# Kernel tuning notes

Hardware: AMD Instinct MI355X
Metric: run time of the kernel (lower is better)

## Reference

```python
import jax, jax.numpy as jnp
import numpy as np

# --- problem-size constants (uniform instance of the ragged structure) ---
B = 64            # claims
EVI = 5           # evidence sequences per claim
SEQS = B * EVI    # total PLM sequences
L = 256           # tokens per sequence
D = 768           # in_channels (PLM hidden)
WORDS = 32        # word-nodes per evidence
TPW = 4           # token refs averaged per word (word_select mean)
N = B * EVI * WORDS   # total graph nodes = 10240
E = N * 16            # edges
R = 4                 # num_relations
DOUT = 768            # out_channels
LH = 1024             # linear_hidden_channels
NC = 3                # num_class


def setup_inputs() -> dict:
    key = jax.random.key(0)
    ks = jax.random.split(key, 16)
    s = 0.02
    return {
        "token_feats": jax.random.normal(ks[0], (SEQS, L, D), jnp.float32),
        "concat_cls": jax.random.normal(ks[1], (B, D), jnp.float32),
        "W_rel1": jax.random.normal(ks[2], (R, D, D), jnp.float32) * s,
        "W_root1": jax.random.normal(ks[3], (D, D), jnp.float32) * s,
        "b1": jnp.zeros((D,), jnp.float32),
        "W_rel2": jax.random.normal(ks[4], (R, D, DOUT), jnp.float32) * s,
        "W_root2": jax.random.normal(ks[5], (D, DOUT), jnp.float32) * s,
        "b2": jnp.zeros((DOUT,), jnp.float32),
        "att_w0": jax.random.normal(ks[6], (D + 2 * DOUT, DOUT), jnp.float32) * s,
        "att_w1": jax.random.normal(ks[7], (DOUT, 1), jnp.float32) * s,
        "lin1_w": jax.random.normal(ks[8], (2 * DOUT + D, LH), jnp.float32) * s,
        "lin1_b": jnp.zeros((LH,), jnp.float32),
        "lin2_w": jax.random.normal(ks[9], (LH, NC), jnp.float32) * s,
        "lin2_b": jnp.zeros((NC,), jnp.float32),
        "word_token_idx": jax.random.randint(ks[10], (N * TPW,), 0, SEQS * L),
        "edge_index": jax.random.randint(ks[11], (2, E), 0, N),
        "edge_type": jax.random.randint(ks[12], (E,), 0, R),
        "claim_seq_idx": jnp.arange(B) * EVI,  # first sequence of each claim
    }


def _rgcn(x, edge_index, edge_type, W_rel, W_root, b):
    # PyG RGCNConv with mean aggregation per relation + root transform + bias
    xr = jnp.einsum('nd,rde->rne', x, W_rel)        # [R, N, Dout]
    src, dst = edge_index[0], edge_index[1]
    msg = xr[edge_type, src]                        # [E, Dout]
    seg = dst * R + edge_type                       # (target, relation) buckets
    cnt = jax.ops.segment_sum(jnp.ones((E,), x.dtype), seg, num_segments=N * R)
    msg = msg / jnp.maximum(cnt, 1.0)[seg][:, None]
    agg = jax.ops.segment_sum(msg, dst, num_segments=N)
    return agg + x @ W_root + b


def reference(token_feats, concat_cls, W_rel1, W_root1, b1, W_rel2, W_root2, b2,
              att_w0, att_w1, lin1_w, lin1_b, lin2_w, lin2_b,
              word_token_idx, edge_index, edge_type, claim_seq_idx):
    # word_select: mean of token vectors per word-node (TPW uniform here)
    tok = token_feats.reshape(-1, D)
    x = tok[word_token_idx].reshape(N, TPW, D).mean(axis=1)       # [N, D]
    claim_cls = token_feats[claim_seq_idx, 0, :]                  # [B, D]

    # 2 RGCN layers with ReLU
    x = jax.nn.relu(_rgcn(x, edge_index, edge_type, W_rel1, W_root1, b1))
    x = jax.nn.relu(_rgcn(x, edge_index, edge_type, W_rel2, W_root2, b2))

    # per-evidence mean||max pooling over its words (uniform WORDS per evidence)
    xe = x.reshape(B * EVI, WORDS, DOUT)
    ev = jnp.concatenate([xe.mean(axis=1), xe.max(axis=1)], axis=-1)  # [B*EVI, 2*Dout]

    # attention scores per evidence, conditioned on the claim CLS
    cc = jnp.repeat(claim_cls, EVI, axis=0)                       # [B*EVI, D]
    h = jax.nn.relu(jnp.concatenate([cc, ev], axis=-1) @ att_w0)
    p = h @ att_w1                                                # [B*EVI, 1]

    # per-claim softmax over its evidences, weighted sum of evidence reps
    a = jax.nn.softmax(p.reshape(B, EVI), axis=1)
    graph = jnp.einsum('be,bed->bd', a, ev.reshape(B, EVI, 2 * DOUT))  # [B, 2*Dout]

    rep = jnp.concatenate([graph, concat_cls], axis=-1)           # [B, 2*Dout + D]
    # dropout is identity in eval mode
    out = jax.nn.log_softmax(jax.nn.relu(rep @ lin1_w + lin1_b) @ lin2_w + lin2_b, axis=-1)
    attention = jax.nn.sigmoid(p[:, 0])                           # [B*EVI]
    return out, attention
```

## Files before the change

### kernel.cpp

```cpp
#include <hip/hip_runtime.h>
#include <hip/hip_fp16.h>


#define BN 64
#define EVI 5
#define SEQS (BN * EVI)
#define LSEQ 256
#define DIM 768
#define WORDS 32
#define TPW 4
#define NNODE (BN * EVI * WORDS)
#define NEDGE (NNODE * 16)
#define RREL 4
#define DOUT 768
#define LH 1024
#define NCLS 3
#define KBIG (5 * DIM)
#define KATT (DIM + 2 * DOUT)

typedef float f32x4 __attribute__((ext_vector_type(4)));
typedef __bf16 bf16x8 __attribute__((ext_vector_type(8)));
typedef unsigned short u16x4 __attribute__((ext_vector_type(4)));

__device__ inline unsigned short f2bf(float f) {
    union { float f; unsigned int u; } v; v.f = f;
    unsigned int u = v.u;
    unsigned int lsb = (u >> 16) & 1u;
    u += 0x7fffu + lsb;
    return (unsigned short)(u >> 16);
}
__device__ inline float bf2f(unsigned short h) {
    union { float f; unsigned int u; } v; v.u = ((unsigned int)h) << 16; return v.f;
}

__device__ inline float ldin(const void* p, long i, int f) {
    if (f == 1) return __half2float(((const __half*)p)[i]);
    if (f == 2) return bf2f(((const unsigned short*)p)[i]);
    return ((const float*)p)[i];
}

__global__ void detect_kernel(const void* w, int* flag) {
    const int lane = threadIdx.x;
    const unsigned int* u32 = (const unsigned int*)w;
    const unsigned short* u16 = (const unsigned short*)w;
    int tiny = 0;
    for (int i = lane; i < 2048; i += 64) {
        unsigned int b = u32[i];
        float f; __builtin_memcpy(&f, &b, 4);
        float a = fabsf(f);
        if (!(a > 1e-10f)) tiny++;
    }
    int band = 0;
    for (int i = lane; i < 4096; i += 64) {
        unsigned short h = u16[i];
        int e8 = (h >> 7) & 0xFF;
        if (h == 0 || (e8 >= 0x66 && e8 <= 0x86)) band++;
    }
#pragma unroll
    for (int o = 32; o > 0; o >>= 1) {
        tiny += __shfl_down(tiny, o);
        band += __shfl_down(band, o);
    }
    if (lane == 0) {
        if (tiny > 1024) { *flag = 1; return; }
        *flag = (band > 3900) ? 2 : 0;
    }
}

__global__ void convert_kernel(const void* __restrict__ src, float* __restrict__ dst,
                               long n, const int* __restrict__ flag)
{
    int f = *flag;
    long stride = (long)gridDim.x * 256;
    for (long i = (long)blockIdx.x * 256 + threadIdx.x; i < n; i += stride)
        dst[i] = ldin(src, i, f);
}

__global__ __launch_bounds__(256) void gather_mean_kernel(
    const void* __restrict__ tok, const int* __restrict__ widx,
    unsigned short* __restrict__ xb, const int* __restrict__ flag)
{
    int f = *flag;
    int n = blockIdx.x;
    long i0 = widx[n * 4 + 0], i1 = widx[n * 4 + 1];
    long i2 = widx[n * 4 + 2], i3 = widx[n * 4 + 3];
    for (int c = threadIdx.x; c < DIM; c += 256) {
        float s = ldin(tok, i0 * DIM + c, f) + ldin(tok, i1 * DIM + c, f)
                + ldin(tok, i2 * DIM + c, f) + ldin(tok, i3 * DIM + c, f);
        xb[(long)n * DIM + c] = f2bf(s * 0.25f);
    }
}

__global__ void count_kernel(const int* __restrict__ ei, const int* __restrict__ et,
                             int* __restrict__ cnt)
{
    int e = blockIdx.x * 256 + threadIdx.x;
    if (e >= NEDGE) return;
    int dst = ei[NEDGE + e];
    int r = et[e];
    atomicAdd(&cnt[dst * RREL + r], 1);
}

__global__ __launch_bounds__(1024) void scan_kernel(const int* __restrict__ cnt,
                                                    int* __restrict__ offs, int n)
{
    const int CH = (n + 1023) >> 10;
    int tid = threadIdx.x;
    int base = tid * CH;
    int s = 0;
    for (int i = 0; i < CH; i++)
        if (base + i < n) s += cnt[base + i];
    __shared__ int buf[1024];
    buf[tid] = s;
    __syncthreads();
    for (int o = 1; o < 1024; o <<= 1) {
        int t = (tid >= o) ? buf[tid - o] : 0;
        __syncthreads();
        buf[tid] += t;
        __syncthreads();
    }
    int run = (tid == 0) ? 0 : buf[tid - 1];
    if (tid == 0) offs[0] = 0;
    for (int i = 0; i < CH; i++) {
        if (base + i < n) {
            run += cnt[base + i];
            offs[base + i + 1] = run;
        }
    }
}

__global__ void fill_kernel(const int* __restrict__ ei, const int* __restrict__ et,
                            const int* __restrict__ offs, int* __restrict__ cursor,
                            int* __restrict__ sorted)
{
    int e = blockIdx.x * 256 + threadIdx.x;
    if (e >= NEDGE) return;
    int src = ei[e];
    int dst = ei[NEDGE + e];
    int r = et[e];
    int seg = dst * RREL + r;
    int pos = offs[seg] + atomicAdd(&cursor[seg], 1);
    sorted[pos] = src;
}

__global__ __launch_bounds__(768) void aggregate_kernel(
    const unsigned short* __restrict__ xsrc, long xstride,
    const int* __restrict__ offs, const int* __restrict__ sorted,
    unsigned short* __restrict__ A, int write_root)
{
    const int n = blockIdx.x;
    const int t = threadIdx.x;
    const int g = t / 192;
    const int l = t - g * 192;
    const long rs4 = xstride >> 2;
    const u16x4* __restrict__ xs4 = (const u16x4*)xsrc;
    u16x4* __restrict__ Ap = (u16x4*)A;
    const long baseQ = ((long)n * KBIG) >> 2;
    const int s0 = offs[n * RREL + g];
    const int s1 = offs[n * RREL + g + 1];
    const float inv = 1.0f / (float)max(s1 - s0, 1);
    float p0[4] = {0, 0, 0, 0}, p1[4] = {0, 0, 0, 0};
    float p2[4] = {0, 0, 0, 0}, p3[4] = {0, 0, 0, 0};
    int i = s0;
    for (; i + 3 < s1; i += 4) {
        int e0 = sorted[i], e1 = sorted[i + 1], e2 = sorted[i + 2], e3 = sorted[i + 3];
        u16x4 w0 = xs4[(long)e0 * rs4 + l];
        u16x4 w1 = xs4[(long)e1 * rs4 + l];
        u16x4 w2 = xs4[(long)e2 * rs4 + l];
        u16x4 w3 = xs4[(long)e3 * rs4 + l];
#pragma unroll
        for (int c = 0; c < 4; c++) {
            p0[c] += bf2f(w0[c]); p1[c] += bf2f(w1[c]);
            p2[c] += bf2f(w2[c]); p3[c] += bf2f(w3[c]);
        }
    }
    for (; i < s1; i++) {
        int e = sorted[i];
        u16x4 w = xs4[(long)e * rs4 + l];
#pragma unroll
        for (int c = 0; c < 4; c++) p0[c] += bf2f(w[c]);
    }
    u16x4 o;
#pragma unroll
    for (int c = 0; c < 4; c++)
        o[c] = f2bf(((p0[c] + p1[c]) + (p2[c] + p3[c])) * inv);
    Ap[baseQ + g * (DIM / 4) + l] = o;
    if (write_root && t < 192)
        Ap[baseQ + RREL * (DIM / 4) + t] = xs4[(long)n * rs4 + t];
}

__global__ __launch_bounds__(256) void transpose_cast_kernel(
    const void* __restrict__ in, int Ncols,
    unsigned short* __restrict__ out, int outStride, int colOff,
    const int* __restrict__ flag)
{
    int f = *flag;
    __shared__ float t[32][33];
    int kt = blockIdx.x * 32, nt = blockIdx.y * 32;
    int lx = threadIdx.x & 31, ly = threadIdx.x >> 5;
    for (int i = 0; i < 4; i++)
        t[ly + i * 8][lx] = ldin(in, (long)(kt + ly + i * 8) * Ncols + nt + lx, f);
    __syncthreads();
    for (int i = 0; i < 4; i++)
        out[(long)(nt + ly + i * 8) * outStride + colOff + kt + lx] = f2bf(t[lx][ly + i * 8]);
}

__global__ __launch_bounds__(256) void gemm_bt_kernel(
    const unsigned short* __restrict__ A, const unsigned short* __restrict__ Bt,
    int K, const float* __restrict__ bias, int relu,
    float* __restrict__ outF, long strideF,
    unsigned short* __restrict__ outB, long strideB)
{
    __shared__ __align__(16) unsigned short As[128 * 32];
    __shared__ __align__(16) unsigned short Bs[128 * 32];
    const int tid = threadIdx.x;
    const int lane = tid & 63, wv = tid >> 6;
    const int wr = wv >> 1, wc = wv & 1;
    const int lr = lane & 15, q = lane >> 4;
    const long m0 = (long)blockIdx.x * 128, n0 = (long)blockIdx.y * 128;

    f32x4 acc[4][4] = {};

    for (int kt = 0; kt < K; kt += 32) {
#pragma unroll
        for (int i = 0; i < 2; i++) {
            int chunk = i * 256 + tid;
            int row = chunk >> 2, kc = (chunk & 3) * 8;
            const unsigned short* ga = A + (m0 + row) * K + kt + kc;
            const unsigned short* gb = Bt + (n0 + row) * K + kt + kc;
            int ldsbase = (i * 256 + wv * 64) * 8;
            __builtin_amdgcn_global_load_lds(
                (const __attribute__((address_space(1))) void*)ga,
                (__attribute__((address_space(3))) void*)&As[ldsbase], 16, 0, 0);
            __builtin_amdgcn_global_load_lds(
                (const __attribute__((address_space(1))) void*)gb,
                (__attribute__((address_space(3))) void*)&Bs[ldsbase], 16, 0, 0);
        }
        __syncthreads();
        bf16x8 af[4], bfr[4];
#pragma unroll
        for (int i = 0; i < 4; i++)
            af[i] = *(const bf16x8*)&As[(wr * 64 + i * 16 + lr) * 32 + q * 8];
#pragma unroll
        for (int j = 0; j < 4; j++)
            bfr[j] = *(const bf16x8*)&Bs[(wc * 64 + j * 16 + lr) * 32 + q * 8];
#pragma unroll
        for (int i = 0; i < 4; i++)
#pragma unroll
            for (int j = 0; j < 4; j++)
                acc[i][j] = __builtin_amdgcn_mfma_f32_16x16x32_bf16(af[i], bfr[j], acc[i][j], 0, 0, 0);
        __syncthreads();
    }

#pragma unroll
    for (int i = 0; i < 4; i++) {
#pragma unroll
        for (int j = 0; j < 4; j++) {
            long col = n0 + wc * 64 + j * 16 + lr;
            float bv = bias ? bias[col] : 0.0f;
#pragma unroll
            for (int r = 0; r < 4; r++) {
                long row = m0 + wr * 64 + i * 16 + q * 4 + r;
                float v = acc[i][j][r] + bv;
                if (relu) v = fmaxf(v, 0.0f);
                if (outF) outF[row * strideF + col] = v;
                if (outB) outB[row * strideB + col] = f2bf(v);
            }
        }
    }
}

__global__ __launch_bounds__(256) void pool_cc_kernel(
    const float* __restrict__ C2, const void* __restrict__ tok,
    const int* __restrict__ csi, unsigned short* __restrict__ A3,
    float* __restrict__ evF, const int* __restrict__ flag)
{
    int f = *flag;
    int s = blockIdx.x;
    int b = s / EVI;
    long seq = csi[b];
    for (int c = threadIdx.x; c < DIM; c += 256) {
        float mx = -1e30f, sm = 0.0f;
        const float* col = C2 + (long)s * WORDS * DOUT + c;
        for (int w = 0; w < WORDS; w++) {
            float v = col[(long)w * DOUT];
            sm += v;
            mx = fmaxf(mx, v);
        }
        float mean = sm * (1.0f / WORDS);
        evF[(long)s * (2 * DOUT) + c] = mean;
        evF[(long)s * (2 * DOUT) + DOUT + c] = mx;
        A3[(long)s * KATT + c] = f2bf(ldin(tok, seq * LSEQ * DIM + c, f));
        A3[(long)s * KATT + DIM + c] = f2bf(mean);
        A3[(long)s * KATT + DIM + DOUT + c] = f2bf(mx);
    }
}

__global__ __launch_bounds__(256) void att_finish_kernel(
    const float* __restrict__ C3, const void* __restrict__ w1,
    const float* __restrict__ evF, const void* __restrict__ ccls,
    float* __restrict__ out, unsigned short* __restrict__ A4,
    const int* __restrict__ flag)
{
    int f = *flag;
    int b = blockIdx.x;
    int t = threadIdx.x;
    __shared__ float red[256];
    __shared__ float a[EVI];
    __shared__ float psh[EVI];
    for (int e = 0; e < EVI; e++) {
        int s = b * EVI + e;
        float sum = 0.0f;
        for (int k = t; k < DOUT; k += 256)
            sum += C3[(long)s * DOUT + k] * ldin(w1, k, f);
        red[t] = sum;
        __syncthreads();
        for (int o = 128; o > 0; o >>= 1) {
            if (t < o) red[t] += red[t + o];
            __syncthreads();
        }
        if (t == 0) psh[e] = red[0];
        __syncthreads();
    }
    if (t < EVI) out[BN * NCLS + b * EVI + t] = 1.0f / (1.0f + __expf(-psh[t]));
    if (t == 0) {
        float m = -1e30f;
        for (int e = 0; e < EVI; e++) m = fmaxf(m, psh[e]);
        float ssum = 0.0f, ex[EVI];
        for (int e = 0; e < EVI; e++) { ex[e] = __expf(psh[e] - m); ssum += ex[e]; }
        for (int e = 0; e < EVI; e++) a[e] = ex[e] / ssum;
    }
    __syncthreads();
    for (int d = t; d < 2 * DOUT; d += 256) {
        float gg = 0.0f;
        for (int e = 0; e < EVI; e++)
            gg += a[e] * evF[(long)(b * EVI + e) * (2 * DOUT) + d];
        A4[(long)b * KATT + d] = f2bf(gg);
    }
    for (int c = t; c < DIM; c += 256)
        A4[(long)b * KATT + 2 * DOUT + c] = f2bf(ldin(ccls, (long)b * DIM + c, f));
}

__global__ __launch_bounds__(256) void final_kernel(
    const float* __restrict__ C4, const void* __restrict__ w2,
    const void* __restrict__ bb, float* __restrict__ out,
    const int* __restrict__ flag)
{
    int f = *flag;
    int b = blockIdx.x;
    float s0 = 0.0f, s1 = 0.0f, s2 = 0.0f;
    for (int k = threadIdx.x; k < LH; k += 256) {
        float h = C4[(long)b * LH + k];
        s0 += h * ldin(w2, k * NCLS + 0, f);
        s1 += h * ldin(w2, k * NCLS + 1, f);
        s2 += h * ldin(w2, k * NCLS + 2, f);
    }
    __shared__ float r0[256], r1[256], r2[256];
    int t = threadIdx.x;
    r0[t] = s0; r1[t] = s1; r2[t] = s2;
    __syncthreads();
    for (int o = 128; o > 0; o >>= 1) {
        if (t < o) { r0[t] += r0[t + o]; r1[t] += r1[t + o]; r2[t] += r2[t + o]; }
        __syncthreads();
    }
    if (t == 0) {
        float l0 = r0[0] + ldin(bb, 0, f), l1 = r1[0] + ldin(bb, 1, f), l2 = r2[0] + ldin(bb, 2, f);
        float m = fmaxf(l0, fmaxf(l1, l2));
        float lse = logf(__expf(l0 - m) + __expf(l1 - m) + __expf(l2 - m)) + m;
        out[b * NCLS + 0] = l0 - lse;
        out[b * NCLS + 1] = l1 - lse;
        out[b * NCLS + 2] = l2 - lse;
    }
}

extern "C" void kernel_launch(void* const* d_in, const int* in_sizes, int n_in,
                              void* d_out, int out_size, void* d_ws, size_t ws_size,
                              hipStream_t stream)
{
    const void* tok      = d_in[0];
    const void* ccls_r   = d_in[1];
    const void* W_rel1_r = d_in[2];
    const void* W_root1_r= d_in[3];
    const void* b1_r     = d_in[4];
    const void* W_rel2_r = d_in[5];
    const void* W_root2_r= d_in[6];
    const void* b2_r     = d_in[7];
    const void* att_w0_r = d_in[8];
    const void* att_w1_r = d_in[9];
    const void* lin1_w_r = d_in[10];
    const void* lin1_b_r = d_in[11];
    const void* lin2_w_r = d_in[12];
    const void* lin2_b_r = d_in[13];
    const int* widx      = (const int*)d_in[14];
    const int* ei        = (const int*)d_in[15];
    const int* et        = (const int*)d_in[16];
    const int* csi       = (const int*)d_in[17];
    float* out           = (float*)d_out;

    char* ws = (char*)d_ws;
    size_t off = 0;
    auto alloc = [&](size_t bytes) { size_t o = off; off = (off + bytes + 255) & ~(size_t)255; return o; };

    int* flag   = (int*)(ws + alloc(256));
    float* b1F     = (float*)(ws + alloc((size_t)DIM * 4));
    float* b2F     = (float*)(ws + alloc((size_t)DOUT * 4));
    float* l1bF    = (float*)(ws + alloc((size_t)LH * 4));
    unsigned short* xb  = (unsigned short*)(ws + alloc((size_t)NNODE * DIM * 2));
    unsigned short* A1  = (unsigned short*)(ws + alloc((size_t)NNODE * KBIG * 2));
    unsigned short* X1  = (unsigned short*)(ws + alloc((size_t)NNODE * DOUT * 2));
    unsigned short* Wt1 = (unsigned short*)(ws + alloc((size_t)DIM * KBIG * 2));
    unsigned short* Wt2 = (unsigned short*)(ws + alloc((size_t)DIM * KBIG * 2));
    unsigned short* Wt3 = (unsigned short*)(ws + alloc((size_t)DOUT * KATT * 2));
    unsigned short* Wt4 = (unsigned short*)(ws + alloc((size_t)LH * KATT * 2));
    float* C2           = (float*)(ws + alloc((size_t)NNODE * DOUT * 4));
    unsigned short* A3  = (unsigned short*)(ws + alloc((size_t)384 * KATT * 2));
    float* C3           = (float*)(ws + alloc((size_t)384 * DOUT * 4));
    float* evF          = (float*)(ws + alloc((size_t)SEQS * 2 * DOUT * 4));
    unsigned short* A4  = (unsigned short*)(ws + alloc((size_t)128 * KATT * 2));
    float* C4           = (float*)(ws + alloc((size_t)128 * LH * 4));
    int* cnt            = (int*)(ws + alloc((size_t)2 * NNODE * RREL * 4));
    int* cursor         = cnt + NNODE * RREL;
    int* offs           = (int*)(ws + alloc((size_t)(NNODE * RREL + 1) * 4));
    int* sorted         = (int*)(ws + alloc((size_t)NEDGE * 4));
    (void)ws_size; (void)in_sizes; (void)n_in; (void)out_size;

    detect_kernel<<<1, 64, 0, stream>>>(W_rel1_r, flag);
    auto conv = [&](const void* src, float* dst, long n) {
        int grid = (int)min((n + 255) / 256, (long)2048);
        convert_kernel<<<grid, 256, 0, stream>>>(src, dst, n, flag);
    };
    conv(b1_r,     b1F,     DIM);
    conv(b2_r,     b2F,     DOUT);
    conv(lin1_b_r, l1bF,    LH);

    hipMemsetAsync(cnt, 0, (size_t)2 * NNODE * RREL * 4, stream);
    count_kernel<<<NEDGE / 256, 256, 0, stream>>>(ei, et, cnt);
    scan_kernel<<<1, 1024, 0, stream>>>(cnt, offs, NNODE * RREL);
    fill_kernel<<<NEDGE / 256, 256, 0, stream>>>(ei, et, offs, cursor, sorted);

    gather_mean_kernel<<<NNODE, 256, 0, stream>>>(tok, widx, xb, flag);

    transpose_cast_kernel<<<dim3(96, 24), 256, 0, stream>>>(W_rel1_r, DIM, Wt1, KBIG, 0, flag);
    transpose_cast_kernel<<<dim3(24, 24), 256, 0, stream>>>(W_root1_r, DIM, Wt1, KBIG, 4 * DIM, flag);
    transpose_cast_kernel<<<dim3(96, 24), 256, 0, stream>>>(W_rel2_r, DOUT, Wt2, KBIG, 0, flag);
    transpose_cast_kernel<<<dim3(24, 24), 256, 0, stream>>>(W_root2_r, DOUT, Wt2, KBIG, 4 * DIM, flag);
    transpose_cast_kernel<<<dim3(72, 24), 256, 0, stream>>>(att_w0_r, DOUT, Wt3, KATT, 0, flag);
    transpose_cast_kernel<<<dim3(72, 32), 256, 0, stream>>>(lin1_w_r, LH, Wt4, KATT, 0, flag);

    aggregate_kernel<<<NNODE, 768, 0, stream>>>(xb, DIM, offs, sorted, A1, 1);
    gemm_bt_kernel<<<dim3(NNODE / 128, DIM / 128), 256, 0, stream>>>(
        A1, Wt1, KBIG, b1F, 1, nullptr, 0, X1, DOUT);

    aggregate_kernel<<<NNODE, 768, 0, stream>>>(X1, DOUT, offs, sorted, A1, 1);
    gemm_bt_kernel<<<dim3(NNODE / 128, DOUT / 128), 256, 0, stream>>>(
        A1, Wt2, KBIG, b2F, 1, C2, DOUT, nullptr, 0);

    pool_cc_kernel<<<SEQS, 256, 0, stream>>>(C2, tok, csi, A3, evF, flag);
    gemm_bt_kernel<<<dim3(3, DOUT / 128), 256, 0, stream>>>(
        A3, Wt3, KATT, nullptr, 1, C3, DOUT, nullptr, 0);
    att_finish_kernel<<<BN, 256, 0, stream>>>(C3, att_w1_r, evF, ccls_r, out, A4, flag);

    gemm_bt_kernel<<<dim3(1, LH / 128), 256, 0, stream>>>(
        A4, Wt4, KATT, l1bF, 1, C4, LH, nullptr, 0);
    final_kernel<<<BN, 256, 0, stream>>>(C4, lin2_w_r, lin2_b_r, out, flag);
}
```

Baseline: 950.0 us.

## Batch weight transposes, split GEMM A operand, widen K tile, vectorize gather

Several changes land together. The three bias conversions and the six weight transpose launches are each merged into a single batched launch, which cuts launch overhead. The root-feature copy into the aggregate buffer is dropped; the GEMM now reads the root part of K directly from the node feature matrix through a second A pointer, saving a write and a read of one fifth of A. The GEMM K tile grows from 32 to 64, halving barrier count at the cost of doubled LDS use. gather_mean now uses one thread per 4 channels with float4 loads on the fp32 path.

```diff
diff --git a/kernel.cpp b/kernel.cpp
--- a/kernel.cpp
+++ b/kernel.cpp
@@ -15,6 +15,7 @@
 #define DOUT 768
 #define LH 1024
 #define NCLS 3
+#define KAGG (4 * DIM)
 #define KBIG (5 * DIM)
 #define KATT (DIM + 2 * DOUT)
 
@@ -67,28 +68,47 @@
     }
 }
 
-__global__ void convert_kernel(const void* __restrict__ src, float* __restrict__ dst,
-                               long n, const int* __restrict__ flag)
-{
-    int f = *flag;
-    long stride = (long)gridDim.x * 256;
-    for (long i = (long)blockIdx.x * 256 + threadIdx.x; i < n; i += stride)
-        dst[i] = ldin(src, i, f);
-}
-
-__global__ __launch_bounds__(256) void gather_mean_kernel(
+__global__ void convert3_kernel(const void* __restrict__ b1, const void* __restrict__ b2,
+                                const void* __restrict__ l1b,
+                                float* __restrict__ b1F, float* __restrict__ b2F,
+                                float* __restrict__ l1bF, const int* __restrict__ flag)
+{
+    int f = *flag;
+    int i = blockIdx.x * 256 + threadIdx.x;
+    if (i < DIM) b1F[i] = ldin(b1, i, f);
+    else if (i < 2 * DIM) b2F[i - DIM] = ldin(b2, i - DIM, f);
+    else if (i < 2 * DIM + LH) l1bF[i - 2 * DIM] = ldin(l1b, i - 2 * DIM, f);
+}
+
+__global__ __launch_bounds__(192) void gather_mean_kernel(
     const void* __restrict__ tok, const int* __restrict__ widx,
     unsigned short* __restrict__ xb, const int* __restrict__ flag)
 {
     int f = *flag;
     int n = blockIdx.x;
+    int t = threadIdx.x;
     long i0 = widx[n * 4 + 0], i1 = widx[n * 4 + 1];
     long i2 = widx[n * 4 + 2], i3 = widx[n * 4 + 3];
-    for (int c = threadIdx.x; c < DIM; c += 256) {
-        float s = ldin(tok, i0 * DIM + c, f) + ldin(tok, i1 * DIM + c, f)
-                + ldin(tok, i2 * DIM + c, f) + ldin(tok, i3 * DIM + c, f);
-        xb[(long)n * DIM + c] = f2bf(s * 0.25f);
-    }
+    u16x4 o;
+    if (f == 0) {
+        const f32x4* tf = (const f32x4*)tok;
+        f32x4 a = tf[i0 * (DIM / 4) + t];
+        f32x4 b = tf[i1 * (DIM / 4) + t];
+        f32x4 c = tf[i2 * (DIM / 4) + t];
+        f32x4 d = tf[i3 * (DIM / 4) + t];
+#pragma unroll
+        for (int c4 = 0; c4 < 4; c4++)
+            o[c4] = f2bf((a[c4] + b[c4] + c[c4] + d[c4]) * 0.25f);
+    } else {
+#pragma unroll
+        for (int c4 = 0; c4 < 4; c4++) {
+            long c = (long)t * 4 + c4;
+            float s = ldin(tok, i0 * DIM + c, f) + ldin(tok, i1 * DIM + c, f)
+                    + ldin(tok, i2 * DIM + c, f) + ldin(tok, i3 * DIM + c, f);
+            o[c4] = f2bf(s * 0.25f);
+        }
+    }
+    ((u16x4*)xb)[(long)n * (DIM / 4) + t] = o;
 }
 
 __global__ void count_kernel(const int* __restrict__ ei, const int* __restrict__ et,
@@ -146,7 +166,7 @@
 __global__ __launch_bounds__(768) void aggregate_kernel(
     const unsigned short* __restrict__ xsrc, long xstride,
     const int* __restrict__ offs, const int* __restrict__ sorted,
-    unsigned short* __restrict__ A, int write_root)
+    unsigned short* __restrict__ A)
 {
     const int n = blockIdx.x;
     const int t = threadIdx.x;
@@ -155,7 +175,7 @@
     const long rs4 = xstride >> 2;
     const u16x4* __restrict__ xs4 = (const u16x4*)xsrc;
     u16x4* __restrict__ Ap = (u16x4*)A;
-    const long baseQ = ((long)n * KBIG) >> 2;
+    const long baseQ = ((long)n * KAGG) >> 2;
     const int s0 = offs[n * RREL + g];
     const int s1 = offs[n * RREL + g + 1];
     const float inv = 1.0f / (float)max(s1 - s0, 1);
@@ -185,34 +205,45 @@
     for (int c = 0; c < 4; c++)
         o[c] = f2bf(((p0[c] + p1[c]) + (p2[c] + p3[c])) * inv);
     Ap[baseQ + g * (DIM / 4) + l] = o;
-    if (write_root && t < 192)
-        Ap[baseQ + RREL * (DIM / 4) + t] = xs4[(long)n * rs4 + t];
-}
-
-__global__ __launch_bounds__(256) void transpose_cast_kernel(
-    const void* __restrict__ in, int Ncols,
-    unsigned short* __restrict__ out, int outStride, int colOff,
+}
+
+__global__ __launch_bounds__(256) void transpose_batch_kernel(
+    const void* __restrict__ s0, const void* __restrict__ s1,
+    const void* __restrict__ s2, const void* __restrict__ s3,
+    const void* __restrict__ s4, const void* __restrict__ s5,
+    unsigned short* __restrict__ Wt1, unsigned short* __restrict__ Wt2,
+    unsigned short* __restrict__ Wt3, unsigned short* __restrict__ Wt4,
     const int* __restrict__ flag)
 {
     int f = *flag;
+    int b = blockIdx.x;
+    const void* src; unsigned short* dst;
+    int Ncols, ostride, coff, ktiles, rel;
+    if (b < 2304)      { src = s0; dst = Wt1; Ncols = DIM;  ostride = KBIG; coff = 0;    ktiles = 96; rel = b; }
+    else if (b < 2880) { src = s1; dst = Wt1; Ncols = DIM;  ostride = KBIG; coff = KAGG; ktiles = 24; rel = b - 2304; }
+    else if (b < 5184) { src = s2; dst = Wt2; Ncols = DOUT; ostride = KBIG; coff = 0;    ktiles = 96; rel = b - 2880; }
+    else if (b < 5760) { src = s3; dst = Wt2; Ncols = DOUT; ostride = KBIG; coff = KAGG; ktiles = 24; rel = b - 5184; }
+    else if (b < 7488) { src = s4; dst = Wt3; Ncols = DOUT; ostride = KATT; coff = 0;    ktiles = 72; rel = b - 5760; }
+    else               { src = s5; dst = Wt4; Ncols = LH;   ostride = KATT; coff = 0;    ktiles = 72; rel = b - 7488; }
+    int kt = (rel % ktiles) * 32, nt = (rel / ktiles) * 32;
     __shared__ float t[32][33];
-    int kt = blockIdx.x * 32, nt = blockIdx.y * 32;
     int lx = threadIdx.x & 31, ly = threadIdx.x >> 5;
     for (int i = 0; i < 4; i++)
-        t[ly + i * 8][lx] = ldin(in, (long)(kt + ly + i * 8) * Ncols + nt + lx, f);
+        t[ly + i * 8][lx] = ldin(src, (long)(kt + ly + i * 8) * Ncols + nt + lx, f);
     __syncthreads();
     for (int i = 0; i < 4; i++)
-        out[(long)(nt + ly + i * 8) * outStride + colOff + kt + lx] = f2bf(t[lx][ly + i * 8]);
+        dst[(long)(nt + ly + i * 8) * ostride + coff + kt + lx] = f2bf(t[lx][ly + i * 8]);
 }
 
 __global__ __launch_bounds__(256) void gemm_bt_kernel(
-    const unsigned short* __restrict__ A, const unsigned short* __restrict__ Bt,
-    int K, const float* __restrict__ bias, int relu,
+    const unsigned short* __restrict__ A, const unsigned short* __restrict__ Ar,
+    int K, int ksplit, const unsigned short* __restrict__ Bt,
+    const float* __restrict__ bias, int relu,
     float* __restrict__ outF, long strideF,
     unsigned short* __restrict__ outB, long strideB)
 {
-    __shared__ __align__(16) unsigned short As[128 * 32];
-    __shared__ __align__(16) unsigned short Bs[128 * 32];
+    __shared__ __align__(16) unsigned short As[128 * 64];
+    __shared__ __align__(16) unsigned short Bs[128 * 64];
     const int tid = threadIdx.x;
     const int lane = tid & 63, wv = tid >> 6;
     const int wr = wv >> 1, wc = wv & 1;
@@ -221,34 +252,42 @@
 
     f32x4 acc[4][4] = {};
 
-    for (int kt = 0; kt < K; kt += 32) {
-#pragma unroll
-        for (int i = 0; i < 2; i++) {
+    for (int kt = 0; kt < K; kt += 64) {
+        const unsigned short* Ab;
+        long sA;
+        if (kt < ksplit) { Ab = A + kt; sA = ksplit; }
+        else             { Ab = Ar + (kt - ksplit); sA = K - ksplit; }
+#pragma unroll
+        for (int i = 0; i < 4; i++) {
             int chunk = i * 256 + tid;
-            int row = chunk >> 2, kc = (chunk & 3) * 8;
-            const unsigned short* ga = A + (m0 + row) * K + kt + kc;
+            int row = chunk >> 3, kc = (chunk & 7) * 8;
+            const unsigned short* ga = Ab + (m0 + row) * sA + kc;
             const unsigned short* gb = Bt + (n0 + row) * K + kt + kc;
-            int ldsbase = (i * 256 + wv * 64) * 8;
             __builtin_amdgcn_global_load_lds(
                 (const __attribute__((address_space(1))) void*)ga,
-                (__attribute__((address_space(3))) void*)&As[ldsbase], 16, 0, 0);
+                (__attribute__((address_space(3))) void*)&As[chunk * 8], 16, 0, 0);
             __builtin_amdgcn_global_load_lds(
                 (const __attribute__((address_space(1))) void*)gb,
-                (__attribute__((address_space(3))) void*)&Bs[ldsbase], 16, 0, 0);
-        }
-        __syncthreads();
-        bf16x8 af[4], bfr[4];
-#pragma unroll
-        for (int i = 0; i < 4; i++)
-            af[i] = *(const bf16x8*)&As[(wr * 64 + i * 16 + lr) * 32 + q * 8];
-#pragma unroll
-        for (int j = 0; j < 4; j++)
-            bfr[j] = *(const bf16x8*)&Bs[(wc * 64 + j * 16 + lr) * 32 + q * 8];
-#pragma unroll
-        for (int i = 0; i < 4; i++)
+                (__attribute__((address_space(3))) void*)&Bs[chunk * 8], 16, 0, 0);
+        }
+        __syncthreads();
+        bf16x8 af[2][4], bfr[2][4];
+#pragma unroll
+        for (int s = 0; s < 2; s++) {
+#pragma unroll
+            for (int i = 0; i < 4; i++)
+                af[s][i] = *(const bf16x8*)&As[(wr * 64 + i * 16 + lr) * 64 + s * 32 + q * 8];
 #pragma unroll
             for (int j = 0; j < 4; j++)
-                acc[i][j] = __builtin_amdgcn_mfma_f32_16x16x32_bf16(af[i], bfr[j], acc[i][j], 0, 0, 0);
+                bfr[s][j] = *(const bf16x8*)&Bs[(wc * 64 + j * 16 + lr) * 64 + s * 32 + q * 8];
+        }
+#pragma unroll
+        for (int s = 0; s < 2; s++)
+#pragma unroll
+            for (int i = 0; i < 4; i++)
+#pragma unroll
+                for (int j = 0; j < 4; j++)
+                    acc[i][j] = __builtin_amdgcn_mfma_f32_16x16x32_bf16(af[s][i], bfr[s][j], acc[i][j], 0, 0, 0);
         __syncthreads();
     }
 
@@ -406,7 +445,7 @@
     float* b2F     = (float*)(ws + alloc((size_t)DOUT * 4));
     float* l1bF    = (float*)(ws + alloc((size_t)LH * 4));
     unsigned short* xb  = (unsigned short*)(ws + alloc((size_t)NNODE * DIM * 2));
-    unsigned short* A1  = (unsigned short*)(ws + alloc((size_t)NNODE * KBIG * 2));
+    unsigned short* A1  = (unsigned short*)(ws + alloc((size_t)NNODE * KAGG * 2));
     unsigned short* X1  = (unsigned short*)(ws + alloc((size_t)NNODE * DOUT * 2));
     unsigned short* Wt1 = (unsigned short*)(ws + alloc((size_t)DIM * KBIG * 2));
     unsigned short* Wt2 = (unsigned short*)(ws + alloc((size_t)DIM * KBIG * 2));
@@ -425,42 +464,34 @@
     (void)ws_size; (void)in_sizes; (void)n_in; (void)out_size;
 
     detect_kernel<<<1, 64, 0, stream>>>(W_rel1_r, flag);
-    auto conv = [&](const void* src, float* dst, long n) {
-        int grid = (int)min((n + 255) / 256, (long)2048);
-        convert_kernel<<<grid, 256, 0, stream>>>(src, dst, n, flag);
-    };
-    conv(b1_r,     b1F,     DIM);
-    conv(b2_r,     b2F,     DOUT);
-    conv(lin1_b_r, l1bF,    LH);
+    convert3_kernel<<<(2 * DIM + LH + 255) / 256, 256, 0, stream>>>(
+        b1_r, b2_r, lin1_b_r, b1F, b2F, l1bF, flag);
 
     hipMemsetAsync(cnt, 0, (size_t)2 * NNODE * RREL * 4, stream);
     count_kernel<<<NEDGE / 256, 256, 0, stream>>>(ei, et, cnt);
     scan_kernel<<<1, 1024, 0, stream>>>(cnt, offs, NNODE * RREL);
     fill_kernel<<<NEDGE / 256, 256, 0, stream>>>(ei, et, offs, cursor, sorted);
 
-    gather_mean_kernel<<<NNODE, 256, 0, stream>>>(tok, widx, xb, flag);
-
-    transpose_cast_kernel<<<dim3(96, 24), 256, 0, stream>>>(W_rel1_r, DIM, Wt1, KBIG, 0, flag);
-    transpose_cast_kernel<<<dim3(24, 24), 256, 0, stream>>>(W_root1_r, DIM, Wt1, KBIG, 4 * DIM, flag);
-    transpose_cast_kernel<<<dim3(96, 24), 256, 0, stream>>>(W_rel2_r, DOUT, Wt2, KBIG, 0, flag);
-    transpose_cast_kernel<<<dim3(24, 24), 256, 0, stream>>>(W_root2_r, DOUT, Wt2, KBIG, 4 * DIM, flag);
-    transpose_cast_kernel<<<dim3(72, 24), 256, 0, stream>>>(att_w0_r, DOUT, Wt3, KATT, 0, flag);
-    transpose_cast_kernel<<<dim3(72, 32), 256, 0, stream>>>(lin1_w_r, LH, Wt4, KATT, 0, flag);
-
-    aggregate_kernel<<<NNODE, 768, 0, stream>>>(xb, DIM, offs, sorted, A1, 1);
+    gather_mean_kernel<<<NNODE, 192, 0, stream>>>(tok, widx, xb, flag);
+
+    transpose_batch_kernel<<<9792, 256, 0, stream>>>(
+        W_rel1_r, W_root1_r, W_rel2_r, W_root2_r, att_w0_r, lin1_w_r,
+        Wt1, Wt2, Wt3, Wt4, flag);
+
+    aggregate_kernel<<<NNODE, 768, 0, stream>>>(xb, DIM, offs, sorted, A1);
     gemm_bt_kernel<<<dim3(NNODE / 128, DIM / 128), 256, 0, stream>>>(
-        A1, Wt1, KBIG, b1F, 1, nullptr, 0, X1, DOUT);
-
-    aggregate_kernel<<<NNODE, 768, 0, stream>>>(X1, DOUT, offs, sorted, A1, 1);
+        A1, xb, KBIG, KAGG, Wt1, b1F, 1, nullptr, 0, X1, DOUT);
+
+    aggregate_kernel<<<NNODE, 768, 0, stream>>>(X1, DOUT, offs, sorted, A1);
     gemm_bt_kernel<<<dim3(NNODE / 128, DOUT / 128), 256, 0, stream>>>(
-        A1, Wt2, KBIG, b2F, 1, C2, DOUT, nullptr, 0);
+        A1, X1, KBIG, KAGG, Wt2, b2F, 1, C2, DOUT, nullptr, 0);
 
     pool_cc_kernel<<<SEQS, 256, 0, stream>>>(C2, tok, csi, A3, evF, flag);
     gemm_bt_kernel<<<dim3(3, DOUT / 128), 256, 0, stream>>>(
-        A3, Wt3, KATT, nullptr, 1, C3, DOUT, nullptr, 0);
+        A3, nullptr, KATT, KATT, Wt3, nullptr, 1, C3, DOUT, nullptr, 0);
     att_finish_kernel<<<BN, 256, 0, stream>>>(C3, att_w1_r, evF, ccls_r, out, A4, flag);
 
     gemm_bt_kernel<<<dim3(1, LH / 128), 256, 0, stream>>>(
-        A4, Wt4, KATT, l1bF, 1, C4, LH, nullptr, 0);
+        A4, nullptr, KATT, KATT, Wt4, l1bF, 1, C4, LH, nullptr, 0);
     final_kernel<<<BN, 256, 0, stream>>>(C4, lin2_w_r, lin2_b_r, out, flag);
 }
```

Measured after the change: 923.4 us. 1.03x faster.
